# Optimization experiments

Measured on AMD Instinct MI355X. Metric: run time of the kernel, lower is better.

The kernel has to match this reference:

```python
import jax, jax.numpy as jnp
import numpy as np
import math

B, NH, T, D = 4, 4, 512, 256
MULT = 128
N = MULT * D // NH  # 8192
MAXLEN = 512
THETA = 2 ** 16
SCALE = N ** -0.5


def _cos_sin():
    # freqs with pairwise quantization: 1/theta**(floor(i/2)*2/N)/(2*pi)
    idx = np.arange(N, dtype=np.float32)
    freqs = 1.0 / THETA ** (np.floor(idx / 2.0) * 2.0 / N) / (2.0 * math.pi)
    phases = np.arange(MAXLEN, dtype=np.float32)[:, None] * freqs[None, :]
    angles = (phases % 1.0) * (2.0 * math.pi)
    return jnp.asarray(np.cos(angles), jnp.float32), jnp.asarray(np.sin(angles), jnp.float32)


def setup_inputs() -> dict:
    key = jax.random.key(0)
    k1, k2, k3 = jax.random.split(key, 3)
    Q = jax.random.uniform(k1, (B, NH, T, N), dtype=jnp.float32)  # post-ReLU sparse acts
    V = jax.random.normal(k2, (B, 1, T, D), dtype=jnp.float32)
    state = jax.random.normal(k3, (B, NH, N, D), dtype=jnp.float32) * 0.02
    cos, sin = _cos_sin()
    return {"Q": Q, "V": V, "state": state, "cos": cos, "sin": sin}


def _rope(v, cos, sin):
    # rotate-half with interleaved pairs: (-v_odd, v_even) interleaved back
    v_even = v[..., ::2]
    v_odd = v[..., 1::2]
    v_rot = jnp.stack([-v_odd, v_even], axis=-1).reshape(v.shape)
    return v * cos + v_rot * sin


def reference(Q, V, state, cos, sin):
    # cos/sin: (MAXLEN, N) -> slice first T positions, broadcast over (B, NH)
    QR = _rope(Q, cos[:T], sin[:T])                      # (B, NH, T, N)
    scores = jnp.matmul(QR, jnp.swapaxes(QR, -2, -1)) * SCALE  # (B, NH, T, T)
    causal = jnp.tril(jnp.ones((T, T), dtype=bool), k=-1)      # strictly lower
    scores = jnp.where(causal, scores, 0.0)
    output = jnp.matmul(scores, V)                       # V (B,1,T,D) broadcasts -> (B,NH,T,D)
    output = output + jnp.matmul(QR, state)              # recurrent state contribution
    chunk_state = jnp.matmul(jnp.swapaxes(QR, -2, -1), V) * SCALE  # (B, NH, N, D)
    new_state = state + chunk_state
    return output, new_state
```

## Files before the change

### kernel.cpp

```cpp
#include <hip/hip_runtime.h>
#include <stdint.h>

#define T_ 512
#define D_ 256
#define N_ 8192
#define NHEAD 16
#define SCALE_ 0.011048543456039806f
#define INV2PI 0.15915493667125702f

typedef __attribute__((ext_vector_type(8))) short bf16x8;
typedef __attribute__((ext_vector_type(4))) float f32x4;

__device__ __forceinline__ unsigned short f2bf(float x) {
  union { float f; unsigned u; } v; v.f = x;
  unsigned r = v.u + 0x7fffu + ((v.u >> 16) & 1u);
  return (unsigned short)(r >> 16);
}

__device__ __forceinline__ void async16(const void* g, void* l) {
  __builtin_amdgcn_global_load_lds(
      (const __attribute__((address_space(1))) unsigned int*)g,
      (__attribute__((address_space(3))) unsigned int*)l,
      16, 0, 0);
}

__device__ __forceinline__ void stage_direct(const unsigned short* __restrict__ g,
                                             int ld, unsigned short* lds, int t) {
  const int row = t >> 2, b = t & 3;
  const int g1 = (b ^ ((row >> 1) & 3)) * 8;
  async16(g + (size_t)row * ld + g1, lds + row * 32 + b * 8);
  const int row2 = row + 64;
  const int g2 = (b ^ ((row2 >> 1) & 3)) * 8;
  async16(g + (size_t)row2 * ld + g2, lds + row2 * 32 + b * 8);
}

__device__ __forceinline__ void stage_trans_bf16(const unsigned short* __restrict__ g,
                                                 int ld, unsigned short* lds, int t) {
  const int mn = t & 127, ks = (t >> 7) * 16;
  __attribute__((aligned(16))) unsigned short u[16];
  #pragma unroll
  for (int i = 0; i < 16; i++) u[i] = g[(size_t)(ks + i) * ld + mn];
  *(uint4*)(lds + mn * 40 + ks)     = *(const uint4*)u;
  *(uint4*)(lds + mn * 40 + ks + 8) = *(const uint4*)(u + 8);
}

__device__ __forceinline__ void stage_trans_f32(const float* __restrict__ g,
                                                int ld, unsigned short* lds, int t) {
  const int mn = t & 127, ks = (t >> 7) * 16;
  float f[16];
  #pragma unroll
  for (int i = 0; i < 16; i++) f[i] = g[(size_t)(ks + i) * ld + mn];
  __attribute__((aligned(16))) unsigned short u[16];
  #pragma unroll
  for (int i = 0; i < 16; i++) u[i] = f2bf(f[i]);
  *(uint4*)(lds + mn * 40 + ks)     = *(const uint4*)u;
  *(uint4*)(lds + mn * 40 + ks + 8) = *(const uint4*)(u + 8);
}

__device__ __forceinline__ void stage_sc(const float* __restrict__ g, int gi0, int gk0,
                                         unsigned short* lds, int t) {
  const int row = t >> 2, c8 = (t & 3) * 8;
  #pragma unroll
  for (int rr = 0; rr < 2; rr++) {
    const int r = row + rr * 64;
    const float* p = g + (size_t)r * T_ + c8;
    float4 x = *(const float4*)p, y = *(const float4*)(p + 4);
    float f[8] = {x.x, x.y, x.z, x.w, y.x, y.y, y.z, y.w};
    const int gi = gi0 + r;
    __attribute__((aligned(16))) unsigned short u[8];
    #pragma unroll
    for (int e = 0; e < 8; e++) {
      float v = ((gk0 + c8 + e) < gi) ? f[e] * SCALE_ : 0.f;
      u[e] = f2bf(v);
    }
    *(uint4*)(lds + r * 40 + c8) = *(const uint4*)u;
  }
}

template<bool SWA, bool SWB>
__device__ __forceinline__ void mfma_step(const unsigned short* as, const unsigned short* bs,
                                          int wr, int wc, int lane, f32x4 acc[4][4]) {
  const int j8 = lane >> 4, rl = lane & 15;
  const int swz = (j8 ^ ((rl >> 1) & 3)) * 8;
  const int pad = j8 * 8;
  bf16x8 a[4], b[4];
  #pragma unroll
  for (int i = 0; i < 4; i++) {
    int r = wr * 64 + i * 16 + rl;
    a[i] = SWA ? *(const bf16x8*)(as + r * 32 + swz)
               : *(const bf16x8*)(as + r * 40 + pad);
  }
  #pragma unroll
  for (int j = 0; j < 4; j++) {
    int r = wc * 64 + j * 16 + rl;
    b[j] = SWB ? *(const bf16x8*)(bs + r * 32 + swz)
               : *(const bf16x8*)(bs + r * 40 + pad);
  }
  #pragma unroll
  for (int i = 0; i < 4; i++)
    #pragma unroll
    for (int j = 0; j < 4; j++)
      acc[i][j] = __builtin_amdgcn_mfma_f32_16x16x32_bf16(a[i], b[j], acc[i][j], 0, 0, 0);
}

__global__ __launch_bounds__(256) void rope_kernel(
    const float* __restrict__ Q, unsigned short* __restrict__ QR)
{
  size_t i8 = ((size_t)blockIdx.x * 256 + threadIdx.x) * 8;
  const int t = (int)((i8 >> 13) & (T_ - 1));
  const int n = (int)(i8 & (N_ - 1));
  float q[8];
  *(float4*)q       = *(const float4*)(Q + i8);
  *(float4*)(q + 4) = *(const float4*)(Q + i8 + 4);
  const float ft = (float)t;
  __attribute__((aligned(16))) unsigned short u[8];
  #pragma unroll
  for (int p = 0; p < 4; p++) {
    const int h = (n >> 1) + p;
    float f = exp2f((float)h * (-1.0f / 256.0f)) * INV2PI;
    float r = ft * f;
    r = r - floorf(r);
    float c = __builtin_amdgcn_cosf(r);
    float s = __builtin_amdgcn_sinf(r);
    float ev = q[2 * p], od = q[2 * p + 1];
    u[2 * p]     = f2bf(ev * c - od * s);
    u[2 * p + 1] = f2bf(od * c + ev * s);
  }
  *(uint4*)(QR + i8) = *(const uint4*)u;
}

#define NB_SC 640
#define NB_OP 512
#define NB_NS 2048
#define OUT_STATE_OFF ((size_t)NHEAD * T_ * D_)

__global__ __launch_bounds__(256) void mega_kernel(
    const unsigned short* __restrict__ QR, const float* __restrict__ V,
    const float* __restrict__ state, float* __restrict__ ScF,
    float* __restrict__ Out)
{
  __shared__ unsigned short as[128 * 40];
  __shared__ unsigned short bs[128 * 40];
  const int blk = blockIdx.x, t = threadIdx.x;
  const int lane = t & 63, w = t >> 6, wr = w >> 1, wc = w & 1;
  const int q4 = (lane >> 4) * 4, rl = lane & 15;
  f32x4 acc[4][4];
  #pragma unroll
  for (int i = 0; i < 4; i++)
    #pragma unroll
    for (int j = 0; j < 4; j++) acc[i][j] = (f32x4){0.f, 0.f, 0.f, 0.f};

  if (blk < NB_SC) {
    static const int TI[10] = {0,1,1,2,2,2,3,3,3,3};
    static const int TJ[10] = {0,0,1,0,1,2,0,1,2,3};
    const int tile = blk >> 2, split = blk & 3;
    const int head = tile / 10, ti = TI[tile % 10], tj = TJ[tile % 10];
    const unsigned short* A  = QR + (size_t)head * T_ * N_ + (size_t)ti * 128 * N_;
    const unsigned short* Bp = QR + (size_t)head * T_ * N_ + (size_t)tj * 128 * N_;
    const int kbeg = split * 2048, kend = kbeg + 2048;
    for (int k0 = kbeg; k0 < kend; k0 += 32) {
      stage_direct(A + k0, N_, as, t);
      stage_direct(Bp + k0, N_, bs, t);
      __syncthreads();
      mfma_step<true, true>(as, bs, wr, wc, lane, acc);
      __syncthreads();
    }
    float* op = ScF + (size_t)head * T_ * T_;
    #pragma unroll
    for (int i = 0; i < 4; i++)
      #pragma unroll
      for (int j = 0; j < 4; j++)
        #pragma unroll
        for (int r = 0; r < 4; r++) {
          int gi = ti * 128 + wr * 64 + i * 16 + q4 + r;
          int gj = tj * 128 + wc * 64 + j * 16 + rl;
          unsafeAtomicAdd(op + (size_t)gi * T_ + gj, acc[i][j][r]);
        }
  } else if (blk < NB_SC + NB_OP) {
    const int idx = blk - NB_SC;
    const int tile = idx >> 2, split = idx & 3;
    const int head = tile >> 3, mt = (tile & 7) >> 1, nt = tile & 1;
    const unsigned short* A = QR + (size_t)head * T_ * N_ + (size_t)mt * 128 * N_;
    const float* Bp = state + (size_t)head * N_ * D_ + nt * 128;
    const int kbeg = split * 2048, kend = kbeg + 2048;
    for (int k0 = kbeg; k0 < kend; k0 += 32) {
      stage_direct(A + k0, N_, as, t);
      stage_trans_f32(Bp + (size_t)k0 * D_, D_, bs, t);
      __syncthreads();
      mfma_step<true, false>(as, bs, wr, wc, lane, acc);
      __syncthreads();
    }
    float* op = Out + (size_t)head * T_ * D_;
    #pragma unroll
    for (int i = 0; i < 4; i++)
      #pragma unroll
      for (int j = 0; j < 4; j++)
        #pragma unroll
        for (int r = 0; r < 4; r++) {
          int gi = mt * 128 + wr * 64 + i * 16 + q4 + r;
          int gj = nt * 128 + wc * 64 + j * 16 + rl;
          unsafeAtomicAdd(op + (size_t)gi * D_ + gj, acc[i][j][r]);
        }
  } else {
    const int idx = blk - (NB_SC + NB_OP);
    const int head = idx >> 7, mt = (idx & 127) >> 1, nt = idx & 1;
    const unsigned short* Asrc = QR + (size_t)head * T_ * N_ + mt * 128;
    const float* Bp = V + (size_t)(head >> 2) * T_ * D_ + nt * 128;
    for (int k0 = 0; k0 < T_; k0 += 32) {
      stage_trans_bf16(Asrc + (size_t)k0 * N_, N_, as, t);
      stage_trans_f32(Bp + (size_t)k0 * D_, D_, bs, t);
      __syncthreads();
      mfma_step<false, false>(as, bs, wr, wc, lane, acc);
      __syncthreads();
    }
    const float* st = state + (size_t)head * N_ * D_;
    float* op = Out + OUT_STATE_OFF + (size_t)head * N_ * D_;
    #pragma unroll
    for (int i = 0; i < 4; i++)
      #pragma unroll
      for (int j = 0; j < 4; j++)
        #pragma unroll
        for (int r = 0; r < 4; r++) {
          int gm = mt * 128 + wr * 64 + i * 16 + q4 + r;
          int gd = nt * 128 + wc * 64 + j * 16 + rl;
          size_t off = (size_t)gm * D_ + gd;
          op[off] = st[off] + SCALE_ * acc[i][j][r];
        }
  }
}

__global__ __launch_bounds__(256) void final_kernel(
    const float* __restrict__ ScF, const float* __restrict__ V,
    float* __restrict__ Out)
{
  __shared__ unsigned short as[128 * 40];
  __shared__ unsigned short bs[128 * 40];
  const int blk = blockIdx.x, t = threadIdx.x;
  const int lane = t & 63, w = t >> 6, wr = w >> 1, wc = w & 1;
  const int q4 = (lane >> 4) * 4, rl = lane & 15;
  const int tile = blk >> 1, split = blk & 1;
  const int head = tile >> 3, mt = (tile & 7) >> 1, nt = tile & 1;
  const float* A = ScF + (size_t)head * T_ * T_ + (size_t)mt * 128 * T_;
  const float* Bp = V + (size_t)(head >> 2) * T_ * D_ + nt * 128;
  f32x4 acc[4][4];
  #pragma unroll
  for (int i = 0; i < 4; i++)
    #pragma unroll
    for (int j = 0; j < 4; j++) acc[i][j] = (f32x4){0.f, 0.f, 0.f, 0.f};
  const int kbeg = split * 256, kend = kbeg + 256;
  for (int k0 = kbeg; k0 < kend; k0 += 32) {
    stage_sc(A + k0, mt * 128, k0, as, t);
    stage_trans_f32(Bp + (size_t)k0 * D_, D_, bs, t);
    __syncthreads();
    mfma_step<false, false>(as, bs, wr, wc, lane, acc);
    __syncthreads();
  }
  float* op = Out + (size_t)head * T_ * D_;
  #pragma unroll
  for (int i = 0; i < 4; i++)
    #pragma unroll
    for (int j = 0; j < 4; j++)
      #pragma unroll
      for (int r = 0; r < 4; r++) {
        int gi = mt * 128 + wr * 64 + i * 16 + q4 + r;
        int gj = nt * 128 + wc * 64 + j * 16 + rl;
        unsafeAtomicAdd(op + (size_t)gi * D_ + gj, acc[i][j][r]);
      }
}

extern "C" void kernel_launch(void* const* d_in, const int* in_sizes, int n_in,
                              void* d_out, int out_size, void* d_ws, size_t ws_size,
                              hipStream_t stream) {
  const float* Q     = (const float*)d_in[0];
  const float* V     = (const float*)d_in[1];
  const float* state = (const float*)d_in[2];
  float* out = (float*)d_out;

  unsigned short* QR = (unsigned short*)d_ws;
  float* ScF = (float*)((char*)d_ws + (size_t)NHEAD * T_ * N_ * 2);

  hipMemsetAsync(ScF, 0, (size_t)NHEAD * T_ * T_ * 4, stream);
  hipMemsetAsync(out, 0, (size_t)NHEAD * T_ * D_ * 4, stream);
  rope_kernel<<<dim3(32768), dim3(256), 0, stream>>>(Q, QR);
  mega_kernel<<<dim3(NB_SC + NB_OP + NB_NS), dim3(256), 0, stream>>>(QR, V, state, ScF, out);
  final_kernel<<<dim3(256), dim3(256), 0, stream>>>(ScF, V, out);
}
```

Before: 796.8 us.

## Pre-transpose QR, state and V to bf16 K-contiguous layouts for direct staging

Adds transpose kernels that write QR^T, state^T (converted to bf16) and V^T (converted to bf16) into workspace. The GEMM branches can then stage both operands with contiguous direct loads instead of strided fp32 transposing loads, and the LDS tiles lose their padding. The cost is extra passes over QR (~134MB) and state, plus a workspace-size requirement. When the workspace is too small it falls back to the old path.

```diff
diff --git a/kernel.cpp b/kernel.cpp
--- a/kernel.cpp
+++ b/kernel.cpp
@@ -129,18 +129,76 @@
   *(uint4*)(QR + i8) = *(const uint4*)u;
 }
 
+__global__ __launch_bounds__(256) void trans_bf16(
+    const unsigned short* __restrict__ src, unsigned short* __restrict__ dst,
+    int R, int C)
+{
+  __shared__ unsigned short tile[64][72];
+  const int t = threadIdx.x;
+  const int r0 = blockIdx.x * 64, c0 = blockIdx.y * 64;
+  src += (size_t)blockIdx.z * R * C;
+  dst += (size_t)blockIdx.z * R * C;
+  #pragma unroll
+  for (int p = 0; p < 2; p++) {
+    int slot = t + p * 256;
+    int row = slot >> 3, c8 = (slot & 7) * 8;
+    *(uint4*)(&tile[row][c8]) =
+        *(const uint4*)(src + (size_t)(r0 + row) * C + c0 + c8);
+  }
+  __syncthreads();
+  #pragma unroll
+  for (int p = 0; p < 2; p++) {
+    int slot = t + p * 256;
+    int n = slot & 63, r8 = (slot >> 6) * 8;
+    __attribute__((aligned(16))) unsigned short u[8];
+    #pragma unroll
+    for (int i = 0; i < 8; i++) u[i] = tile[r8 + i][n];
+    *(uint4*)(dst + (size_t)(c0 + n) * R + r0 + r8) = *(const uint4*)u;
+  }
+}
+
+__global__ __launch_bounds__(256) void trans_f32_bf16(
+    const float* __restrict__ src, unsigned short* __restrict__ dst,
+    int R, int C)
+{
+  __shared__ unsigned short tile[64][72];
+  const int t = threadIdx.x;
+  const int r0 = blockIdx.x * 64, c0 = blockIdx.y * 64;
+  src += (size_t)blockIdx.z * R * C;
+  dst += (size_t)blockIdx.z * R * C;
+  #pragma unroll
+  for (int p = 0; p < 4; p++) {
+    int slot = t + p * 256;
+    int row = slot >> 4, c4 = (slot & 15) * 4;
+    float4 v = *(const float4*)(src + (size_t)(r0 + row) * C + c0 + c4);
+    __attribute__((aligned(8))) unsigned short u[4] =
+        {f2bf(v.x), f2bf(v.y), f2bf(v.z), f2bf(v.w)};
+    *(uint2*)(&tile[row][c4]) = *(const uint2*)u;
+  }
+  __syncthreads();
+  #pragma unroll
+  for (int p = 0; p < 2; p++) {
+    int slot = t + p * 256;
+    int n = slot & 63, r8 = (slot >> 6) * 8;
+    __attribute__((aligned(16))) unsigned short u[8];
+    #pragma unroll
+    for (int i = 0; i < 8; i++) u[i] = tile[r8 + i][n];
+    *(uint4*)(dst + (size_t)(c0 + n) * R + r0 + r8) = *(const uint4*)u;
+  }
+}
+
 #define NB_SC 640
 #define NB_OP 512
 #define NB_NS 2048
 #define OUT_STATE_OFF ((size_t)NHEAD * T_ * D_)
 
-__global__ __launch_bounds__(256) void mega_kernel(
-    const unsigned short* __restrict__ QR, const float* __restrict__ V,
-    const float* __restrict__ state, float* __restrict__ ScF,
-    float* __restrict__ Out)
-{
-  __shared__ unsigned short as[128 * 40];
-  __shared__ unsigned short bs[128 * 40];
+__global__ __launch_bounds__(256) void mega2_kernel(
+    const unsigned short* __restrict__ QR, const unsigned short* __restrict__ QRT,
+    const unsigned short* __restrict__ STT, const unsigned short* __restrict__ VT,
+    const float* __restrict__ state, float* __restrict__ ScF, float* __restrict__ Out)
+{
+  __shared__ unsigned short as[128 * 32];
+  __shared__ unsigned short bs[128 * 32];
   const int blk = blockIdx.x, t = threadIdx.x;
   const int lane = t & 63, w = t >> 6, wr = w >> 1, wc = w & 1;
   const int q4 = (lane >> 4) * 4, rl = lane & 15;
@@ -180,6 +238,140 @@
     const int idx = blk - NB_SC;
     const int tile = idx >> 2, split = idx & 3;
     const int head = tile >> 3, mt = (tile & 7) >> 1, nt = tile & 1;
+    const unsigned short* A  = QR  + (size_t)head * T_ * N_ + (size_t)mt * 128 * N_;
+    const unsigned short* Bp = STT + (size_t)head * D_ * N_ + (size_t)nt * 128 * N_;
+    const int kbeg = split * 2048, kend = kbeg + 2048;
+    for (int k0 = kbeg; k0 < kend; k0 += 32) {
+      stage_direct(A + k0, N_, as, t);
+      stage_direct(Bp + k0, N_, bs, t);
+      __syncthreads();
+      mfma_step<true, true>(as, bs, wr, wc, lane, acc);
+      __syncthreads();
+    }
+    float* op = Out + (size_t)head * T_ * D_;
+    #pragma unroll
+    for (int i = 0; i < 4; i++)
+      #pragma unroll
+      for (int j = 0; j < 4; j++)
+        #pragma unroll
+        for (int r = 0; r < 4; r++) {
+          int gi = mt * 128 + wr * 64 + i * 16 + q4 + r;
+          int gj = nt * 128 + wc * 64 + j * 16 + rl;
+          unsafeAtomicAdd(op + (size_t)gi * D_ + gj, acc[i][j][r]);
+        }
+  } else {
+    const int idx = blk - (NB_SC + NB_OP);
+    const int head = idx >> 7, mt = (idx & 127) >> 1, nt = idx & 1;
+    const unsigned short* A  = QRT + (size_t)head * N_ * T_ + (size_t)mt * 128 * T_;
+    const unsigned short* Bp = VT + (size_t)(head >> 2) * D_ * T_ + (size_t)nt * 128 * T_;
+    for (int k0 = 0; k0 < T_; k0 += 32) {
+      stage_direct(A + k0, T_, as, t);
+      stage_direct(Bp + k0, T_, bs, t);
+      __syncthreads();
+      mfma_step<true, true>(as, bs, wr, wc, lane, acc);
+      __syncthreads();
+    }
+    const float* st = state + (size_t)head * N_ * D_;
+    float* op = Out + OUT_STATE_OFF + (size_t)head * N_ * D_;
+    #pragma unroll
+    for (int i = 0; i < 4; i++)
+      #pragma unroll
+      for (int j = 0; j < 4; j++)
+        #pragma unroll
+        for (int r = 0; r < 4; r++) {
+          int gm = mt * 128 + wr * 64 + i * 16 + q4 + r;
+          int gd = nt * 128 + wc * 64 + j * 16 + rl;
+          size_t off = (size_t)gm * D_ + gd;
+          op[off] = st[off] + SCALE_ * acc[i][j][r];
+        }
+  }
+}
+
+__global__ __launch_bounds__(256) void final2_kernel(
+    const float* __restrict__ ScF, const unsigned short* __restrict__ VT,
+    float* __restrict__ Out)
+{
+  __shared__ unsigned short as[128 * 40];
+  __shared__ unsigned short bs[128 * 32];
+  const int blk = blockIdx.x, t = threadIdx.x;
+  const int lane = t & 63, w = t >> 6, wr = w >> 1, wc = w & 1;
+  const int q4 = (lane >> 4) * 4, rl = lane & 15;
+  const int tile = blk >> 1, split = blk & 1;
+  const int head = tile >> 3, mt = (tile & 7) >> 1, nt = tile & 1;
+  const float* A = ScF + (size_t)head * T_ * T_ + (size_t)mt * 128 * T_;
+  const unsigned short* Bp = VT + (size_t)(head >> 2) * D_ * T_ + (size_t)nt * 128 * T_;
+  f32x4 acc[4][4];
+  #pragma unroll
+  for (int i = 0; i < 4; i++)
+    #pragma unroll
+    for (int j = 0; j < 4; j++) acc[i][j] = (f32x4){0.f, 0.f, 0.f, 0.f};
+  const int kbeg = split * 256, kend = kbeg + 256;
+  for (int k0 = kbeg; k0 < kend; k0 += 32) {
+    stage_sc(A + k0, mt * 128, k0, as, t);
+    stage_direct(Bp + k0, T_, bs, t);
+    __syncthreads();
+    mfma_step<false, true>(as, bs, wr, wc, lane, acc);
+    __syncthreads();
+  }
+  float* op = Out + (size_t)head * T_ * D_;
+  #pragma unroll
+  for (int i = 0; i < 4; i++)
+    #pragma unroll
+    for (int j = 0; j < 4; j++)
+      #pragma unroll
+      for (int r = 0; r < 4; r++) {
+        int gi = mt * 128 + wr * 64 + i * 16 + q4 + r;
+        int gj = nt * 128 + wc * 64 + j * 16 + rl;
+        unsafeAtomicAdd(op + (size_t)gi * D_ + gj, acc[i][j][r]);
+      }
+}
+
+__global__ __launch_bounds__(256) void mega_kernel(
+    const unsigned short* __restrict__ QR, const float* __restrict__ V,
+    const float* __restrict__ state, float* __restrict__ ScF,
+    float* __restrict__ Out)
+{
+  __shared__ unsigned short as[128 * 40];
+  __shared__ unsigned short bs[128 * 40];
+  const int blk = blockIdx.x, t = threadIdx.x;
+  const int lane = t & 63, w = t >> 6, wr = w >> 1, wc = w & 1;
+  const int q4 = (lane >> 4) * 4, rl = lane & 15;
+  f32x4 acc[4][4];
+  #pragma unroll
+  for (int i = 0; i < 4; i++)
+    #pragma unroll
+    for (int j = 0; j < 4; j++) acc[i][j] = (f32x4){0.f, 0.f, 0.f, 0.f};
+
+  if (blk < NB_SC) {
+    static const int TI[10] = {0,1,1,2,2,2,3,3,3,3};
+    static const int TJ[10] = {0,0,1,0,1,2,0,1,2,3};
+    const int tile = blk >> 2, split = blk & 3;
+    const int head = tile / 10, ti = TI[tile % 10], tj = TJ[tile % 10];
+    const unsigned short* A  = QR + (size_t)head * T_ * N_ + (size_t)ti * 128 * N_;
+    const unsigned short* Bp = QR + (size_t)head * T_ * N_ + (size_t)tj * 128 * N_;
+    const int kbeg = split * 2048, kend = kbeg + 2048;
+    for (int k0 = kbeg; k0 < kend; k0 += 32) {
+      stage_direct(A + k0, N_, as, t);
+      stage_direct(Bp + k0, N_, bs, t);
+      __syncthreads();
+      mfma_step<true, true>(as, bs, wr, wc, lane, acc);
+      __syncthreads();
+    }
+    float* op = ScF + (size_t)head * T_ * T_;
+    #pragma unroll
+    for (int i = 0; i < 4; i++)
+      #pragma unroll
+      for (int j = 0; j < 4; j++)
+        #pragma unroll
+        for (int r = 0; r < 4; r++) {
+          int gi = ti * 128 + wr * 64 + i * 16 + q4 + r;
+          int gj = tj * 128 + wc * 64 + j * 16 + rl;
+          unsafeAtomicAdd(op + (size_t)gi * T_ + gj, acc[i][j][r]);
+        }
+  } else if (blk < NB_SC + NB_OP) {
+    const int idx = blk - NB_SC;
+    const int tile = idx >> 2, split = idx & 3;
+    const int head = tile >> 3, mt = (tile & 7) >> 1, nt = tile & 1;
     const unsigned short* A = QR + (size_t)head * T_ * N_ + (size_t)mt * 128 * N_;
     const float* Bp = state + (size_t)head * N_ * D_ + nt * 128;
     const int kbeg = split * 2048, kend = kbeg + 2048;
@@ -268,6 +460,12 @@
       }
 }
 
+#define SCF_OFF  ((size_t)134217728)
+#define QRT_OFF  ((size_t)150994944)
+#define STT_OFF  ((size_t)285212672)
+#define VT_OFF   ((size_t)352321536)
+#define WS_NEED  ((size_t)353370112)
+
 extern "C" void kernel_launch(void* const* d_in, const int* in_sizes, int n_in,
                               void* d_out, int out_size, void* d_ws, size_t ws_size,
                               hipStream_t stream) {
@@ -277,11 +475,24 @@
   float* out = (float*)d_out;
 
   unsigned short* QR = (unsigned short*)d_ws;
-  float* ScF = (float*)((char*)d_ws + (size_t)NHEAD * T_ * N_ * 2);
+  float* ScF = (float*)((char*)d_ws + SCF_OFF);
 
   hipMemsetAsync(ScF, 0, (size_t)NHEAD * T_ * T_ * 4, stream);
   hipMemsetAsync(out, 0, (size_t)NHEAD * T_ * D_ * 4, stream);
   rope_kernel<<<dim3(32768), dim3(256), 0, stream>>>(Q, QR);
-  mega_kernel<<<dim3(NB_SC + NB_OP + NB_NS), dim3(256), 0, stream>>>(QR, V, state, ScF, out);
-  final_kernel<<<dim3(256), dim3(256), 0, stream>>>(ScF, V, out);
-}
+
+  if (ws_size >= WS_NEED) {
+    unsigned short* QRT = (unsigned short*)((char*)d_ws + QRT_OFF);
+    unsigned short* STT = (unsigned short*)((char*)d_ws + STT_OFF);
+    unsigned short* VTp = (unsigned short*)((char*)d_ws + VT_OFF);
+    trans_bf16    <<<dim3(8, 128, 16), dim3(256), 0, stream>>>(QR, QRT, T_, N_);
+    trans_f32_bf16<<<dim3(128, 4, 16), dim3(256), 0, stream>>>(state, STT, N_, D_);
+    trans_f32_bf16<<<dim3(8, 4, 4),    dim3(256), 0, stream>>>(V, VTp, T_, D_);
+    mega2_kernel<<<dim3(NB_SC + NB_OP + NB_NS), dim3(256), 0, stream>>>(
+        QR, QRT, STT, VTp, state, ScF, out);
+    final2_kernel<<<dim3(256), dim3(256), 0, stream>>>(ScF, VTp, out);
+  } else {
+    mega_kernel<<<dim3(NB_SC + NB_OP + NB_NS), dim3(256), 0, stream>>>(QR, V, state, ScF, out);
+    final_kernel<<<dim3(256), dim3(256), 0, stream>>>(ScF, V, out);
+  }
+}
```

New measurement: 854.4 us. +7.2%, slower.

## Pre-transpose QR, state and V to bf16 so GEMMs use async direct loads

Applied to the files above, without the earlier changes.

The RoPE kernel now also writes a transposed bf16 copy of QR through an LDS tile. Separate transpose kernels convert state and V to transposed bf16 layouts. The main GEMM phases can then use async global-to-LDS loads with swizzled tiles, replacing strided per-element transposing loads. Block indices in the mega kernel are also interleaved across the three work types. The cost is extra workspace, an extra pass over state and Q-derived data, and more kernel launches.

```diff
diff --git a/kernel.cpp b/kernel.cpp
--- a/kernel.cpp
+++ b/kernel.cpp
@@ -34,29 +34,6 @@
   async16(g + (size_t)row2 * ld + g2, lds + row2 * 32 + b * 8);
 }
 
-__device__ __forceinline__ void stage_trans_bf16(const unsigned short* __restrict__ g,
-                                                 int ld, unsigned short* lds, int t) {
-  const int mn = t & 127, ks = (t >> 7) * 16;
-  __attribute__((aligned(16))) unsigned short u[16];
-  #pragma unroll
-  for (int i = 0; i < 16; i++) u[i] = g[(size_t)(ks + i) * ld + mn];
-  *(uint4*)(lds + mn * 40 + ks)     = *(const uint4*)u;
-  *(uint4*)(lds + mn * 40 + ks + 8) = *(const uint4*)(u + 8);
-}
-
-__device__ __forceinline__ void stage_trans_f32(const float* __restrict__ g,
-                                                int ld, unsigned short* lds, int t) {
-  const int mn = t & 127, ks = (t >> 7) * 16;
-  float f[16];
-  #pragma unroll
-  for (int i = 0; i < 16; i++) f[i] = g[(size_t)(ks + i) * ld + mn];
-  __attribute__((aligned(16))) unsigned short u[16];
-  #pragma unroll
-  for (int i = 0; i < 16; i++) u[i] = f2bf(f[i]);
-  *(uint4*)(lds + mn * 40 + ks)     = *(const uint4*)u;
-  *(uint4*)(lds + mn * 40 + ks + 8) = *(const uint4*)(u + 8);
-}
-
 __device__ __forceinline__ void stage_sc(const float* __restrict__ g, int gi0, int gk0,
                                          unsigned short* lds, int t) {
   const int row = t >> 2, c8 = (t & 3) * 8;
@@ -103,45 +80,101 @@
       acc[i][j] = __builtin_amdgcn_mfma_f32_16x16x32_bf16(a[i], b[j], acc[i][j], 0, 0, 0);
 }
 
-__global__ __launch_bounds__(256) void rope_kernel(
-    const float* __restrict__ Q, unsigned short* __restrict__ QR)
+__global__ __launch_bounds__(256) void rope2_kernel(
+    const float* __restrict__ Q, unsigned short* __restrict__ QR,
+    unsigned short* __restrict__ QRT)
 {
-  size_t i8 = ((size_t)blockIdx.x * 256 + threadIdx.x) * 8;
-  const int t = (int)((i8 >> 13) & (T_ - 1));
-  const int n = (int)(i8 & (N_ - 1));
-  float q[8];
-  *(float4*)q       = *(const float4*)(Q + i8);
-  *(float4*)(q + 4) = *(const float4*)(Q + i8 + 4);
-  const float ft = (float)t;
-  __attribute__((aligned(16))) unsigned short u[8];
+  __shared__ unsigned short tile[64][64];
+  const int tid = threadIdx.x;
+  const int n0 = blockIdx.x * 64, t0 = blockIdx.y * 64, h = blockIdx.z;
+  const float* src = Q + ((size_t)h * T_ + t0) * N_ + n0;
   #pragma unroll
   for (int p = 0; p < 4; p++) {
-    const int h = (n >> 1) + p;
-    float f = exp2f((float)h * (-1.0f / 256.0f)) * INV2PI;
-    float r = ft * f;
-    r = r - floorf(r);
-    float c = __builtin_amdgcn_cosf(r);
-    float s = __builtin_amdgcn_sinf(r);
-    float ev = q[2 * p], od = q[2 * p + 1];
-    u[2 * p]     = f2bf(ev * c - od * s);
-    u[2 * p + 1] = f2bf(od * c + ev * s);
-  }
-  *(uint4*)(QR + i8) = *(const uint4*)u;
+    const int slot = tid + p * 256;
+    const int row = slot >> 4, c4 = (slot & 15) * 4;
+    float4 v = *(const float4*)(src + (size_t)row * N_ + c4);
+    const float ft = (float)(t0 + row);
+    __attribute__((aligned(8))) unsigned short u[4];
+    #pragma unroll
+    for (int pp = 0; pp < 2; pp++) {
+      const int m = ((n0 + c4) >> 1) + pp;
+      float f = exp2f((float)m * (-1.0f / 256.0f)) * INV2PI;
+      float r = ft * f;
+      r = r - floorf(r);
+      float cs = __builtin_amdgcn_cosf(r);
+      float sn = __builtin_amdgcn_sinf(r);
+      float ev = (pp == 0) ? v.x : v.z;
+      float od = (pp == 0) ? v.y : v.w;
+      u[2 * pp]     = f2bf(ev * cs - od * sn);
+      u[2 * pp + 1] = f2bf(od * cs + ev * sn);
+    }
+    *(uint2*)(&tile[row][c4 ^ (row & 56)]) = *(const uint2*)u;
+  }
+  __syncthreads();
+  unsigned short* qr = QR + ((size_t)h * T_ + t0) * N_ + n0;
+  #pragma unroll
+  for (int p = 0; p < 2; p++) {
+    const int slot = tid + p * 256;
+    const int row = slot >> 3, c8 = (slot & 7) * 8;
+    *(uint4*)(qr + (size_t)row * N_ + c8) = *(const uint4*)(&tile[row][c8 ^ (row & 56)]);
+  }
+  unsigned short* qrt = QRT + ((size_t)h * N_ + n0) * T_ + t0;
+  #pragma unroll
+  for (int p = 0; p < 2; p++) {
+    const int slot = tid + p * 256;
+    const int n = slot >> 3, r8 = (slot & 7) * 8;
+    __attribute__((aligned(16))) unsigned short u[8];
+    #pragma unroll
+    for (int i = 0; i < 8; i++) u[i] = tile[r8 + i][n ^ r8];
+    *(uint4*)(qrt + (size_t)n * T_ + r8) = *(const uint4*)u;
+  }
+}
+
+__global__ __launch_bounds__(256) void trans2_f32_bf16(
+    const float* __restrict__ src, unsigned short* __restrict__ dst,
+    int R, int C)
+{
+  __shared__ unsigned short tile[64][64];
+  const int tid = threadIdx.x;
+  const int r0 = blockIdx.x * 64, c0 = blockIdx.y * 64;
+  src += (size_t)blockIdx.z * R * C;
+  dst += (size_t)blockIdx.z * R * C;
+  #pragma unroll
+  for (int p = 0; p < 4; p++) {
+    const int slot = tid + p * 256;
+    const int row = slot >> 4, c4 = (slot & 15) * 4;
+    float4 v = *(const float4*)(src + (size_t)(r0 + row) * C + c0 + c4);
+    __attribute__((aligned(8))) unsigned short u[4] =
+        {f2bf(v.x), f2bf(v.y), f2bf(v.z), f2bf(v.w)};
+    *(uint2*)(&tile[row][c4 ^ (row & 56)]) = *(const uint2*)u;
+  }
+  __syncthreads();
+  #pragma unroll
+  for (int p = 0; p < 2; p++) {
+    const int slot = tid + p * 256;
+    const int n = slot >> 3, r8 = (slot & 7) * 8;
+    __attribute__((aligned(16))) unsigned short u[8];
+    #pragma unroll
+    for (int i = 0; i < 8; i++) u[i] = tile[r8 + i][n ^ r8];
+    *(uint4*)(dst + (size_t)(c0 + n) * R + r0 + r8) = *(const uint4*)u;
+  }
 }
 
 #define NB_SC 640
 #define NB_OP 512
 #define NB_NS 2048
+#define NB_TOT (NB_SC + NB_OP + NB_NS)
 #define OUT_STATE_OFF ((size_t)NHEAD * T_ * D_)
 
-__global__ __launch_bounds__(256) void mega_kernel(
-    const unsigned short* __restrict__ QR, const float* __restrict__ V,
-    const float* __restrict__ state, float* __restrict__ ScF,
-    float* __restrict__ Out)
+__global__ __launch_bounds__(256) void mega2_kernel(
+    const unsigned short* __restrict__ QR, const unsigned short* __restrict__ QRT,
+    const unsigned short* __restrict__ STT, const unsigned short* __restrict__ VT,
+    const float* __restrict__ state, float* __restrict__ ScF, float* __restrict__ Out)
 {
-  __shared__ unsigned short as[128 * 40];
-  __shared__ unsigned short bs[128 * 40];
-  const int blk = blockIdx.x, t = threadIdx.x;
+  __shared__ unsigned short as[128 * 32];
+  __shared__ unsigned short bs[128 * 32];
+  const int blk = (blockIdx.x & 7) * (NB_TOT / 8) + (blockIdx.x >> 3);
+  const int t = threadIdx.x;
   const int lane = t & 63, w = t >> 6, wr = w >> 1, wc = w & 1;
   const int q4 = (lane >> 4) * 4, rl = lane & 15;
   f32x4 acc[4][4];
@@ -180,14 +213,14 @@
     const int idx = blk - NB_SC;
     const int tile = idx >> 2, split = idx & 3;
     const int head = tile >> 3, mt = (tile & 7) >> 1, nt = tile & 1;
-    const unsigned short* A = QR + (size_t)head * T_ * N_ + (size_t)mt * 128 * N_;
-    const float* Bp = state + (size_t)head * N_ * D_ + nt * 128;
+    const unsigned short* A  = QR  + (size_t)head * T_ * N_ + (size_t)mt * 128 * N_;
+    const unsigned short* Bp = STT + (size_t)head * D_ * N_ + (size_t)nt * 128 * N_;
     const int kbeg = split * 2048, kend = kbeg + 2048;
     for (int k0 = kbeg; k0 < kend; k0 += 32) {
       stage_direct(A + k0, N_, as, t);
-      stage_trans_f32(Bp + (size_t)k0 * D_, D_, bs, t);
-      __syncthreads();
-      mfma_step<true, false>(as, bs, wr, wc, lane, acc);
+      stage_direct(Bp + k0, N_, bs, t);
+      __syncthreads();
+      mfma_step<true, true>(as, bs, wr, wc, lane, acc);
       __syncthreads();
     }
     float* op = Out + (size_t)head * T_ * D_;
@@ -204,13 +237,13 @@
   } else {
     const int idx = blk - (NB_SC + NB_OP);
     const int head = idx >> 7, mt = (idx & 127) >> 1, nt = idx & 1;
-    const unsigned short* Asrc = QR + (size_t)head * T_ * N_ + mt * 128;
-    const float* Bp = V + (size_t)(head >> 2) * T_ * D_ + nt * 128;
+    const unsigned short* A  = QRT + (size_t)head * N_ * T_ + (size_t)mt * 128 * T_;
+    const unsigned short* Bp = VT + (size_t)(head >> 2) * D_ * T_ + (size_t)nt * 128 * T_;
     for (int k0 = 0; k0 < T_; k0 += 32) {
-      stage_trans_bf16(Asrc + (size_t)k0 * N_, N_, as, t);
-      stage_trans_f32(Bp + (size_t)k0 * D_, D_, bs, t);
-      __syncthreads();
-      mfma_step<false, false>(as, bs, wr, wc, lane, acc);
+      stage_direct(A + k0, T_, as, t);
+      stage_direct(Bp + k0, T_, bs, t);
+      __syncthreads();
+      mfma_step<true, true>(as, bs, wr, wc, lane, acc);
       __syncthreads();
     }
     const float* st = state + (size_t)head * N_ * D_;
@@ -229,19 +262,19 @@
   }
 }
 
-__global__ __launch_bounds__(256) void final_kernel(
-    const float* __restrict__ ScF, const float* __restrict__ V,
+__global__ __launch_bounds__(256) void final2_kernel(
+    const float* __restrict__ ScF, const unsigned short* __restrict__ VT,
     float* __restrict__ Out)
 {
   __shared__ unsigned short as[128 * 40];
-  __shared__ unsigned short bs[128 * 40];
+  __shared__ unsigned short bs[128 * 32];
   const int blk = blockIdx.x, t = threadIdx.x;
   const int lane = t & 63, w = t >> 6, wr = w >> 1, wc = w & 1;
   const int q4 = (lane >> 4) * 4, rl = lane & 15;
   const int tile = blk >> 1, split = blk & 1;
   const int head = tile >> 3, mt = (tile & 7) >> 1, nt = tile & 1;
   const float* A = ScF + (size_t)head * T_ * T_ + (size_t)mt * 128 * T_;
-  const float* Bp = V + (size_t)(head >> 2) * T_ * D_ + nt * 128;
+  const unsigned short* Bp = VT + (size_t)(head >> 2) * D_ * T_ + (size_t)nt * 128 * T_;
   f32x4 acc[4][4];
   #pragma unroll
   for (int i = 0; i < 4; i++)
@@ -250,9 +283,9 @@
   const int kbeg = split * 256, kend = kbeg + 256;
   for (int k0 = kbeg; k0 < kend; k0 += 32) {
     stage_sc(A + k0, mt * 128, k0, as, t);
-    stage_trans_f32(Bp + (size_t)k0 * D_, D_, bs, t);
+    stage_direct(Bp + k0, T_, bs, t);
     __syncthreads();
-    mfma_step<false, false>(as, bs, wr, wc, lane, acc);
+    mfma_step<false, true>(as, bs, wr, wc, lane, acc);
     __syncthreads();
   }
   float* op = Out + (size_t)head * T_ * D_;
@@ -268,6 +301,11 @@
       }
 }
 
+#define SCF_OFF  ((size_t)134217728)
+#define QRT_OFF  ((size_t)150994944)
+#define STT_OFF  ((size_t)285212672)
+#define VT_OFF   ((size_t)352321536)
+
 extern "C" void kernel_launch(void* const* d_in, const int* in_sizes, int n_in,
                               void* d_out, int out_size, void* d_ws, size_t ws_size,
                               hipStream_t stream) {
@@ -276,12 +314,17 @@
   const float* state = (const float*)d_in[2];
   float* out = (float*)d_out;
 
-  unsigned short* QR = (unsigned short*)d_ws;
-  float* ScF = (float*)((char*)d_ws + (size_t)NHEAD * T_ * N_ * 2);
+  unsigned short* QR  = (unsigned short*)d_ws;
+  float* ScF          = (float*)((char*)d_ws + SCF_OFF);
+  unsigned short* QRT = (unsigned short*)((char*)d_ws + QRT_OFF);
+  unsigned short* STT = (unsigned short*)((char*)d_ws + STT_OFF);
+  unsigned short* VTp = (unsigned short*)((char*)d_ws + VT_OFF);
 
   hipMemsetAsync(ScF, 0, (size_t)NHEAD * T_ * T_ * 4, stream);
   hipMemsetAsync(out, 0, (size_t)NHEAD * T_ * D_ * 4, stream);
-  rope_kernel<<<dim3(32768), dim3(256), 0, stream>>>(Q, QR);
-  mega_kernel<<<dim3(NB_SC + NB_OP + NB_NS), dim3(256), 0, stream>>>(QR, V, state, ScF, out);
-  final_kernel<<<dim3(256), dim3(256), 0, stream>>>(ScF, V, out);
-}
+  rope2_kernel<<<dim3(128, 8, 16), dim3(256), 0, stream>>>(Q, QR, QRT);
+  trans2_f32_bf16<<<dim3(128, 4, 16), dim3(256), 0, stream>>>(state, STT, N_, D_);
+  trans2_f32_bf16<<<dim3(8, 4, 4),    dim3(256), 0, stream>>>(V, VTp, T_, D_);
+  mega2_kernel<<<dim3(NB_TOT), dim3(256), 0, stream>>>(QR, QRT, STT, VTp, state, ScF, out);
+  final2_kernel<<<dim3(256), dim3(256), 0, stream>>>(ScF, VTp, out);
+}
```

After: 948.7 us. 19.1% more time.
